# Kernel tuning notes

Measured on AMD Instinct MI355X. Metric: run time of the kernel, lower is better.

Reference implementation:

```python
import jax, jax.numpy as jnp
import numpy as np

TOP_K = 2


def setup_inputs() -> dict:
    key = jax.random.key(0)
    ks = jax.random.split(key, 8)
    B, S, D, E = 4, 2048, 768, 8
    F = 4 * D
    scale = 0.02
    x = jax.random.normal(ks[0], (B, S, D), dtype=jnp.float32)
    router_w = jax.random.normal(ks[1], (D, E), dtype=jnp.float32) * scale
    router_b = jnp.zeros((E,), dtype=jnp.float32)
    w1 = jax.random.normal(ks[2], (E, D, F), dtype=jnp.float32) * scale
    b1 = jnp.zeros((E, F), dtype=jnp.float32)
    w2 = jax.random.normal(ks[3], (E, F, D), dtype=jnp.float32) * scale
    b2 = jnp.zeros((E, D), dtype=jnp.float32)
    return {"x": x, "router_w": router_w, "router_b": router_b,
            "w1": w1, "b1": b1, "w2": w2, "b2": b2}


def reference(x, router_w, router_b, w1, b1, w2, b2):
    E = w1.shape[0]
    # router: [B,S,E]
    logits = jnp.einsum('bsd,de->bse', x, router_w) + router_b
    probs = jax.nn.softmax(logits, axis=-1)
    top_p, top_i = jax.lax.top_k(probs, TOP_K)          # [B,S,K]
    top_p = top_p / jnp.sum(top_p, axis=-1, keepdims=True)
    # dense combine weights [B,S,E]: renormalized top-k prob if selected else 0
    combine = jnp.sum(jax.nn.one_hot(top_i, E, dtype=x.dtype) * top_p[..., None], axis=-2)
    # loop over small fixed expert count (structurally distinct weight slices)
    out = jnp.zeros_like(x)
    for e in range(E):
        h = jax.nn.gelu(jnp.einsum('bsd,df->bsf', x, w1[e]) + b1[e], approximate=False)
        y = jnp.einsum('bsf,fd->bsd', h, w2[e]) + b2[e]
        out = out + combine[..., e:e + 1] * y
    return out
```

## Files before the change

### kernel.cpp

```cpp
#include <hip/hip_runtime.h>
#include <hip/hip_bf16.h>
#include <math.h>

#define TOKENS 8192
#define Dm 768
#define Fm 3072
#define Em 8
#define BK 64

typedef __attribute__((ext_vector_type(8))) short short8v;
typedef __attribute__((ext_vector_type(4))) short short4v;
typedef __attribute__((ext_vector_type(4))) float f32x4;

__device__ inline short f2b(float f) {
  __hip_bfloat16 h = __float2bfloat16(f);
  return *reinterpret_cast<short*>(&h);
}

__device__ inline void async16(short* lds, const short* g) {
  __builtin_amdgcn_global_load_lds((const __attribute__((address_space(1))) void*)g,
                                   (__attribute__((address_space(3))) void*)lds, 16, 0, 0);
}

__global__ __launch_bounds__(256) void cvt_tr_kernel(const float* __restrict__ in,
                                                     short* __restrict__ out, int R, int C) {
  __shared__ short tile[64][68];
  size_t eoff = (size_t)blockIdx.z * R * C;
  const float* inp = in + eoff;
  short* outp = out + eoff;
  int tc = blockIdx.x * 64, tr = blockIdx.y * 64;
  {
    int row = threadIdx.x >> 2;
    int cch = (threadIdx.x & 3) * 16;
    const float* src = inp + (size_t)(tr + row) * C + tc + cch;
    #pragma unroll
    for (int q = 0; q < 4; q++) {
      float4 v = *(const float4*)(src + q * 4);
      tile[row][cch + q * 4 + 0] = f2b(v.x);
      tile[row][cch + q * 4 + 1] = f2b(v.y);
      tile[row][cch + q * 4 + 2] = f2b(v.z);
      tile[row][cch + q * 4 + 3] = f2b(v.w);
    }
  }
  __syncthreads();
  {
    int c = threadIdx.x >> 2;
    int rch = (threadIdx.x & 3) * 16;
    short tmp[16];
    #pragma unroll
    for (int i = 0; i < 16; i++) tmp[i] = tile[rch + i][c];
    short* dst = outp + (size_t)(tc + c) * R + tr + rch;
    *(short8v*)(dst) = *(short8v*)(tmp);
    *(short8v*)(dst + 8) = *(short8v*)(tmp + 8);
  }
}

__global__ __launch_bounds__(256) void router_kernel(
    const float* __restrict__ x, const float* __restrict__ rw,
    const float* __restrict__ rb, short* __restrict__ xb,
    int2* __restrict__ meta_e, float2* __restrict__ meta_p) {
  int wave = threadIdx.x >> 6;
  int lane = threadIdx.x & 63;
  int t = blockIdx.x * 4 + wave;
  if (t >= TOKENS) return;
  const float* xr = x + (size_t)t * Dm;
  short* xbr = xb + (size_t)t * Dm;
  float acc[Em];
  #pragma unroll
  for (int e = 0; e < Em; e++) acc[e] = 0.f;
  #pragma unroll
  for (int i = 0; i < 3; i++) {
    int d = i * 256 + lane * 4;
    float4 v = *(const float4*)(xr + d);
    short4v s;
    s[0] = f2b(v.x); s[1] = f2b(v.y); s[2] = f2b(v.z); s[3] = f2b(v.w);
    *(short4v*)(xbr + d) = s;
    #pragma unroll
    for (int j = 0; j < 4; j++) {
      float xv = (j == 0) ? v.x : (j == 1) ? v.y : (j == 2) ? v.z : v.w;
      const float4* rwp = (const float4*)(rw + (size_t)(d + j) * Em);
      float4 a = rwp[0], b = rwp[1];
      acc[0] += xv * a.x; acc[1] += xv * a.y; acc[2] += xv * a.z; acc[3] += xv * a.w;
      acc[4] += xv * b.x; acc[5] += xv * b.y; acc[6] += xv * b.z; acc[7] += xv * b.w;
    }
  }
  #pragma unroll
  for (int e = 0; e < Em; e++) {
    float v = acc[e];
    #pragma unroll
    for (int s = 32; s > 0; s >>= 1) v += __shfl_xor(v, s);
    acc[e] = v + rb[e];
  }
  int i1 = 0; float m1 = acc[0];
  #pragma unroll
  for (int e = 1; e < Em; e++) if (acc[e] > m1) { m1 = acc[e]; i1 = e; }
  int i2 = -1; float m2 = -1e30f;
  #pragma unroll
  for (int e = 0; e < Em; e++) if (e != i1 && acc[e] > m2) { m2 = acc[e]; i2 = e; }
  float tt = expf(m2 - m1);
  float p0 = 1.f / (1.f + tt);
  float p1 = tt / (1.f + tt);
  if (lane == 0) {
    meta_e[t] = make_int2(i1, i2);
    meta_p[t] = make_float2(p0, p1);
  }
}

__global__ __launch_bounds__(256) void scatter_kernel(
    const int2* __restrict__ meta_e, int* __restrict__ cnt,
    int* __restrict__ list, int4* __restrict__ meta_i) {
  __shared__ int lcnt[Em];
  __shared__ int gbase[Em];
  int t = blockIdx.x * 256 + threadIdx.x;
  if (threadIdx.x < Em) lcnt[threadIdx.x] = 0;
  __syncthreads();
  int2 e = meta_e[t];
  int r0 = atomicAdd(&lcnt[e.x], 1);
  int r1 = atomicAdd(&lcnt[e.y], 1);
  __syncthreads();
  if (threadIdx.x < Em) gbase[threadIdx.x] = atomicAdd(&cnt[threadIdx.x], lcnt[threadIdx.x]);
  __syncthreads();
  int s0 = gbase[e.x] + r0;
  int s1 = gbase[e.y] + r1;
  list[e.x * TOKENS + s0] = t;
  list[e.y * TOKENS + s1] = t;
  meta_i[t] = make_int4(e.x, s0, e.y, s1);
}

__global__ void prefix_kernel(const int* __restrict__ cnt, int* __restrict__ hoffs,
                              int2* __restrict__ table, int* __restrict__ ntab) {
  if (threadIdx.x == 0) {
    int s = 0, k = 0;
    for (int e = 0; e < Em; e++) {
      hoffs[e] = s;
      int c = cnt[e];
      for (int mb = 0; mb < c; mb += 128) table[k++] = make_int2(e, mb);
      s += c;
    }
    ntab[0] = k;
  }
}

template <int MODE>
__global__ __launch_bounds__(256, 3) void moe_gemm_kernel(
    const short* __restrict__ Abase, const short* __restrict__ Wt,
    const float* __restrict__ bias, short* __restrict__ Hout,
    float* __restrict__ Yout, const int* __restrict__ cnt,
    const int* __restrict__ hoffs, const int* __restrict__ list,
    const int2* __restrict__ table, const int* __restrict__ ntab,
    int Ndim, int Kdim) {
  int ti = blockIdx.y;
  if (ti >= ntab[0]) return;
  int2 te = table[ti];
  int e = te.x, mbase = te.y;
  int count = cnt[e], ho = hoffs[e];
  int n0 = blockIdx.x * 128;

  __shared__ short As[128 * 64];
  __shared__ short Bs[128 * 64];
  __shared__ int rid_s[128];

  int tid = threadIdx.x;
  if (MODE == 0) {
    if (tid < 128) {
      int rc = mbase + tid; if (rc > count - 1) rc = count - 1;
      rid_s[tid] = list[e * TOKENS + rc];
    }
  }
  __syncthreads();

  const short* We = Wt + (size_t)e * Ndim * Kdim;
  const short* aptr[4];
  const short* bptr[4];
  #pragma unroll
  for (int q = 0; q < 4; q++) {
    int r = q * 32 + (tid >> 3);
    int g = (tid & 7) ^ (r & 7);
    size_t grow;
    if (MODE == 0) {
      grow = (size_t)rid_s[r] * Kdim;
    } else {
      int rr = mbase + r; if (rr > count - 1) rr = count - 1;
      grow = (size_t)(ho + rr) * Kdim;
    }
    aptr[q] = Abase + grow + g * 8;
    bptr[q] = We + (size_t)(n0 + r) * Kdim + g * 8;
  }
  int w = tid >> 6;
  int NT = Kdim / BK;

  f32x4 acc[4][4] = {};
  int lane = tid & 63;
  int wm = w >> 1, wn = w & 1;
  int lr = lane & 15, lh = lane >> 4;
  int rsw = lr & 7;

  for (int t = 0; t < NT; t++) {
    #pragma unroll
    for (int q = 0; q < 4; q++) {
      async16(&As[q * 2048 + w * 512], aptr[q]); aptr[q] += BK;
      async16(&Bs[q * 2048 + w * 512], bptr[q]); bptr[q] += BK;
    }
    __syncthreads();
    #pragma unroll
    for (int kk = 0; kk < 2; kk++) {
      short8v a[4], b[4];
      #pragma unroll
      for (int m = 0; m < 4; m++)
        a[m] = *(const short8v*)&As[(wm * 64 + m * 16 + lr) * 64 + ((kk * 4 + lh) ^ rsw) * 8];
      #pragma unroll
      for (int n = 0; n < 4; n++)
        b[n] = *(const short8v*)&Bs[(wn * 64 + n * 16 + lr) * 64 + ((kk * 4 + lh) ^ rsw) * 8];
      #pragma unroll
      for (int m = 0; m < 4; m++)
        #pragma unroll
        for (int n = 0; n < 4; n++)
          acc[m][n] = __builtin_amdgcn_mfma_f32_16x16x32_bf16(a[m], b[n], acc[m][n], 0, 0, 0);
    }
    __syncthreads();
  }

  if (MODE == 0) {
    const float* be = bias + (size_t)e * Ndim;
    #pragma unroll
    for (int m = 0; m < 4; m++) {
      #pragma unroll
      for (int j = 0; j < 4; j++) {
        int r = wm * 64 + m * 16 + lh * 4 + j;
        if (mbase + r < count) {
          size_t rowoff = (size_t)(ho + mbase + r) * Ndim;
          #pragma unroll
          for (int n = 0; n < 4; n++) {
            int colg = n0 + wn * 64 + n * 16 + lr;
            float val = acc[m][n][j] + be[colg];
            float z = val * 0.70710678118654752f;
            float az = fabsf(z);
            float tt = __fdividef(1.f, fmaf(0.3275911f, az, 1.f));
            float poly = fmaf(fmaf(fmaf(fmaf(1.061405429f, tt, -1.453152027f), tt,
                              1.421413741f), tt, -0.284496736f), tt, 0.254829592f) * tt;
            float er = 1.f - poly * __expf(-az * az);
            er = z < 0.f ? -er : er;
            val = 0.5f * val * (1.f + er);
            Hout[rowoff + colg] = f2b(val);
          }
        }
      }
    }
  } else {
    #pragma unroll
    for (int m = 0; m < 4; m++) {
      #pragma unroll
      for (int j = 0; j < 4; j++) {
        int r = wm * 64 + m * 16 + lh * 4 + j;
        if (mbase + r < count) {
          float* yrow = Yout + (size_t)(ho + mbase + r) * Ndim;
          #pragma unroll
          for (int n = 0; n < 4; n++) {
            int colg = n0 + wn * 64 + n * 16 + lr;
            yrow[colg] = acc[m][n][j];
          }
        }
      }
    }
  }
}

__global__ __launch_bounds__(256) void combine_kernel(
    const float* __restrict__ Y, const float* __restrict__ b2,
    const int* __restrict__ hoffs, const int4* __restrict__ meta_i,
    const float2* __restrict__ meta_p, float* __restrict__ out) {
  int wave = threadIdx.x >> 6;
  int lane = threadIdx.x & 63;
  int t = blockIdx.x * 4 + wave;
  if (t >= TOKENS) return;
  int4 mi = meta_i[t];
  float2 mp = meta_p[t];
  const float4* y0 = (const float4*)(Y + (size_t)(hoffs[mi.x] + mi.y) * Dm);
  const float4* y1 = (const float4*)(Y + (size_t)(hoffs[mi.z] + mi.w) * Dm);
  const float4* ba = (const float4*)(b2 + (size_t)mi.x * Dm);
  const float4* bb = (const float4*)(b2 + (size_t)mi.z * Dm);
  float4* orow = (float4*)(out + (size_t)t * Dm);
  #pragma unroll
  for (int i = 0; i < 3; i++) {
    int idx = lane + 64 * i;
    float4 v0 = y0[idx], v1 = y1[idx], a = ba[idx], b = bb[idx];
    float4 o;
    o.x = mp.x * (v0.x + a.x) + mp.y * (v1.x + b.x);
    o.y = mp.x * (v0.y + a.y) + mp.y * (v1.y + b.y);
    o.z = mp.x * (v0.z + a.z) + mp.y * (v1.z + b.z);
    o.w = mp.x * (v0.w + a.w) + mp.y * (v1.w + b.w);
    orow[idx] = o;
  }
}

extern "C" void kernel_launch(void* const* d_in, const int* in_sizes, int n_in,
                              void* d_out, int out_size, void* d_ws, size_t ws_size,
                              hipStream_t stream) {
  const float* x  = (const float*)d_in[0];
  const float* rw = (const float*)d_in[1];
  const float* rb = (const float*)d_in[2];
  const float* w1 = (const float*)d_in[3];
  const float* b1 = (const float*)d_in[4];
  const float* w2 = (const float*)d_in[5];
  const float* b2 = (const float*)d_in[6];
  float* out = (float*)d_out;
  char* ws = (char*)d_ws;

  const size_t off_cnt    = 0;
  const size_t off_hoffs  = 64;
  const size_t off_ntab   = 128;
  const size_t off_table  = 192;
  const size_t off_list   = 2048;
  const size_t off_meta_i = off_list + (size_t)Em * TOKENS * 4;
  const size_t off_meta_p = off_meta_i + (size_t)TOKENS * 16;
  const size_t off_meta_e = off_meta_p + (size_t)TOKENS * 8;
  const size_t off_xbf    = off_meta_e + (size_t)TOKENS * 8;
  const size_t off_w1t    = off_xbf + (size_t)TOKENS * Dm * 2;
  const size_t off_w2t    = off_w1t + (size_t)Em * Dm * Fm * 2;
  const size_t off_h      = off_w2t + (size_t)Em * Fm * Dm * 2;
  const size_t needed     = off_h + (size_t)2 * TOKENS * Fm * 2;
  if (ws_size < needed) return;

  int*    cnt    = (int*)(ws + off_cnt);
  int*    hoffs  = (int*)(ws + off_hoffs);
  int*    ntab   = (int*)(ws + off_ntab);
  int2*   table  = (int2*)(ws + off_table);
  int*    list   = (int*)(ws + off_list);
  int4*   meta_i = (int4*)(ws + off_meta_i);
  float2* meta_p = (float2*)(ws + off_meta_p);
  int2*   meta_e = (int2*)(ws + off_meta_e);
  short*  xbf    = (short*)(ws + off_xbf);
  short*  w1t    = (short*)(ws + off_w1t);
  short*  w2t    = (short*)(ws + off_w2t);
  short*  h      = (short*)(ws + off_h);
  float*  y      = (float*)(ws + off_xbf);

  hipMemsetAsync(cnt, 0, 32, stream);
  cvt_tr_kernel<<<dim3(Fm / 64, Dm / 64, Em), 256, 0, stream>>>(w1, w1t, Dm, Fm);
  cvt_tr_kernel<<<dim3(Dm / 64, Fm / 64, Em), 256, 0, stream>>>(w2, w2t, Fm, Dm);
  router_kernel<<<TOKENS / 4, 256, 0, stream>>>(x, rw, rb, xbf, meta_e, meta_p);
  scatter_kernel<<<TOKENS / 256, 256, 0, stream>>>(meta_e, cnt, list, meta_i);
  prefix_kernel<<<1, 64, 0, stream>>>(cnt, hoffs, table, ntab);
  moe_gemm_kernel<0><<<dim3(Fm / 128, 136), 256, 0, stream>>>(
      xbf, w1t, b1, h, nullptr, cnt, hoffs, list, table, ntab, Fm, Dm);
  moe_gemm_kernel<1><<<dim3(Dm / 128, 136), 256, 0, stream>>>(
      h, w2t, nullptr, nullptr, y, cnt, hoffs, list, table, ntab, Dm, Fm);
  combine_kernel<<<TOKENS / 4, 256, 0, stream>>>(y, b2, hoffs, meta_i, meta_p, out);
}
```

Before: 364.0 us.

## Enlarge MoE GEMM tiles, double-buffer LDS, and fuse combine via atomic scatter

Grows the grouped GEMM tile from 128x128 to 256x256 with 512-thread blocks, adds double-buffered async LDS staging, and remaps a 1D grid to spread work across XCDs. The combine kernel is removed. The router pre-writes the bias-weighted output, and the second GEMM atomically adds the probability-weighted results straight into the output rows. This cuts the Y intermediate round-trip and one kernel launch, and raises reuse per tile. It costs fp32 atomics, more padding waste on the larger M tiles, 128 KB of LDS per block, and higher register pressure.

```diff
diff --git a/kernel.cpp b/kernel.cpp
--- a/kernel.cpp
+++ b/kernel.cpp
@@ -7,6 +7,7 @@
 #define Fm 3072
 #define Em 8
 #define BK 64
+#define MT_MAX 71
 
 typedef __attribute__((ext_vector_type(8))) short short8v;
 typedef __attribute__((ext_vector_type(4))) short short4v;
@@ -57,7 +58,8 @@
 
 __global__ __launch_bounds__(256) void router_kernel(
     const float* __restrict__ x, const float* __restrict__ rw,
-    const float* __restrict__ rb, short* __restrict__ xb,
+    const float* __restrict__ rb, const float* __restrict__ b2,
+    short* __restrict__ xb, float* __restrict__ out,
     int2* __restrict__ meta_e, float2* __restrict__ meta_p) {
   int wave = threadIdx.x >> 6;
   int lane = threadIdx.x & 63;
@@ -100,6 +102,18 @@
   float tt = expf(m2 - m1);
   float p0 = 1.f / (1.f + tt);
   float p1 = tt / (1.f + tt);
+  const float4* ba = (const float4*)(b2 + (size_t)i1 * Dm);
+  const float4* bb = (const float4*)(b2 + (size_t)i2 * Dm);
+  float4* orow = (float4*)(out + (size_t)t * Dm);
+  #pragma unroll
+  for (int i = 0; i < 3; i++) {
+    int idx = lane + 64 * i;
+    float4 a = ba[idx], b = bb[idx];
+    float4 o;
+    o.x = p0 * a.x + p1 * b.x; o.y = p0 * a.y + p1 * b.y;
+    o.z = p0 * a.z + p1 * b.z; o.w = p0 * a.w + p1 * b.w;
+    orow[idx] = o;
+  }
   if (lane == 0) {
     meta_e[t] = make_int2(i1, i2);
     meta_p[t] = make_float2(p0, p1);
@@ -107,14 +121,15 @@
 }
 
 __global__ __launch_bounds__(256) void scatter_kernel(
-    const int2* __restrict__ meta_e, int* __restrict__ cnt,
-    int* __restrict__ list, int4* __restrict__ meta_i) {
+    const int2* __restrict__ meta_e, const float2* __restrict__ meta_p,
+    int* __restrict__ cnt, int* __restrict__ list, float* __restrict__ wlist) {
   __shared__ int lcnt[Em];
   __shared__ int gbase[Em];
   int t = blockIdx.x * 256 + threadIdx.x;
   if (threadIdx.x < Em) lcnt[threadIdx.x] = 0;
   __syncthreads();
   int2 e = meta_e[t];
+  float2 p = meta_p[t];
   int r0 = atomicAdd(&lcnt[e.x], 1);
   int r1 = atomicAdd(&lcnt[e.y], 1);
   __syncthreads();
@@ -122,9 +137,8 @@
   __syncthreads();
   int s0 = gbase[e.x] + r0;
   int s1 = gbase[e.y] + r1;
-  list[e.x * TOKENS + s0] = t;
-  list[e.y * TOKENS + s1] = t;
-  meta_i[t] = make_int4(e.x, s0, e.y, s1);
+  list[e.x * TOKENS + s0] = t;  wlist[e.x * TOKENS + s0] = p.x;
+  list[e.y * TOKENS + s1] = t;  wlist[e.y * TOKENS + s1] = p.y;
 }
 
 __global__ void prefix_kernel(const int* __restrict__ cnt, int* __restrict__ hoffs,
@@ -134,38 +148,42 @@
     for (int e = 0; e < Em; e++) {
       hoffs[e] = s;
       int c = cnt[e];
-      for (int mb = 0; mb < c; mb += 128) table[k++] = make_int2(e, mb);
+      for (int mb = 0; mb < c; mb += 256) table[k++] = make_int2(e, mb);
       s += c;
     }
     ntab[0] = k;
   }
 }
 
-template <int MODE>
-__global__ __launch_bounds__(256, 3) void moe_gemm_kernel(
+template <int MODE, int NB>
+__global__ __launch_bounds__(512, 2) void moe_gemm_kernel(
     const short* __restrict__ Abase, const short* __restrict__ Wt,
     const float* __restrict__ bias, short* __restrict__ Hout,
-    float* __restrict__ Yout, const int* __restrict__ cnt,
+    float* __restrict__ Out, const int* __restrict__ cnt,
     const int* __restrict__ hoffs, const int* __restrict__ list,
-    const int2* __restrict__ table, const int* __restrict__ ntab,
-    int Ndim, int Kdim) {
-  int ti = blockIdx.y;
+    const float* __restrict__ wlist, const int2* __restrict__ table,
+    const int* __restrict__ ntab, int Ndim, int Kdim) {
+  int nwg = gridDim.x;
+  int orig = blockIdx.x;
+  int q8 = nwg >> 3, r8 = nwg & 7, xcd = orig & 7;
+  int wg = (xcd < r8 ? xcd * (q8 + 1) : r8 * (q8 + 1) + (xcd - r8) * q8) + (orig >> 3);
+  int ti = wg / NB, nt = wg % NB;
   if (ti >= ntab[0]) return;
   int2 te = table[ti];
   int e = te.x, mbase = te.y;
   int count = cnt[e], ho = hoffs[e];
-  int n0 = blockIdx.x * 128;
-
-  __shared__ short As[128 * 64];
-  __shared__ short Bs[128 * 64];
-  __shared__ int rid_s[128];
+  int n0 = nt * 256;
+
+  __shared__ short As[2][256 * 64];
+  __shared__ short Bs[2][256 * 64];
+  __shared__ int rid_s[256];
+  __shared__ float pw_s[256];
 
   int tid = threadIdx.x;
-  if (MODE == 0) {
-    if (tid < 128) {
-      int rc = mbase + tid; if (rc > count - 1) rc = count - 1;
-      rid_s[tid] = list[e * TOKENS + rc];
-    }
+  if (tid < 256) {
+    int rc = mbase + tid; if (rc > count - 1) rc = count - 1;
+    rid_s[tid] = list[e * TOKENS + rc];
+    pw_s[tid] = wlist[e * TOKENS + rc];
   }
   __syncthreads();
 
@@ -174,7 +192,7 @@
   const short* bptr[4];
   #pragma unroll
   for (int q = 0; q < 4; q++) {
-    int r = q * 32 + (tid >> 3);
+    int r = q * 64 + (tid >> 3);
     int g = (tid & 7) ^ (r & 7);
     size_t grow;
     if (MODE == 0) {
@@ -187,46 +205,57 @@
     bptr[q] = We + (size_t)(n0 + r) * Kdim + g * 8;
   }
   int w = tid >> 6;
+
+  #define STAGE(s)                                             \
+    {                                                          \
+      _Pragma("unroll")                                        \
+      for (int q = 0; q < 4; q++) {                            \
+        async16(&As[s][q * 4096 + w * 512], aptr[q]); aptr[q] += BK; \
+        async16(&Bs[s][q * 4096 + w * 512], bptr[q]); bptr[q] += BK; \
+      }                                                        \
+      __builtin_amdgcn_sched_barrier(0);                       \
+    }
+
   int NT = Kdim / BK;
-
-  f32x4 acc[4][4] = {};
+  f32x4 acc[8][4] = {};
   int lane = tid & 63;
-  int wm = w >> 1, wn = w & 1;
+  int wm = (tid >> 6) >> 2, wn = (tid >> 6) & 3;
   int lr = lane & 15, lh = lane >> 4;
   int rsw = lr & 7;
 
+  STAGE(0);
+  __syncthreads();
   for (int t = 0; t < NT; t++) {
-    #pragma unroll
-    for (int q = 0; q < 4; q++) {
-      async16(&As[q * 2048 + w * 512], aptr[q]); aptr[q] += BK;
-      async16(&Bs[q * 2048 + w * 512], bptr[q]); bptr[q] += BK;
-    }
-    __syncthreads();
+    int cur = t & 1;
+    if (t + 1 < NT) STAGE(cur ^ 1);
+    const short* Ab = As[cur];
+    const short* Bb = Bs[cur];
     #pragma unroll
     for (int kk = 0; kk < 2; kk++) {
-      short8v a[4], b[4];
-      #pragma unroll
-      for (int m = 0; m < 4; m++)
-        a[m] = *(const short8v*)&As[(wm * 64 + m * 16 + lr) * 64 + ((kk * 4 + lh) ^ rsw) * 8];
+      short8v a[8], b[4];
+      #pragma unroll
+      for (int m = 0; m < 8; m++)
+        a[m] = *(const short8v*)&Ab[(wm * 128 + m * 16 + lr) * 64 + ((kk * 4 + lh) ^ rsw) * 8];
       #pragma unroll
       for (int n = 0; n < 4; n++)
-        b[n] = *(const short8v*)&Bs[(wn * 64 + n * 16 + lr) * 64 + ((kk * 4 + lh) ^ rsw) * 8];
-      #pragma unroll
-      for (int m = 0; m < 4; m++)
+        b[n] = *(const short8v*)&Bb[(wn * 64 + n * 16 + lr) * 64 + ((kk * 4 + lh) ^ rsw) * 8];
+      #pragma unroll
+      for (int m = 0; m < 8; m++)
         #pragma unroll
         for (int n = 0; n < 4; n++)
           acc[m][n] = __builtin_amdgcn_mfma_f32_16x16x32_bf16(a[m], b[n], acc[m][n], 0, 0, 0);
     }
     __syncthreads();
   }
+  #undef STAGE
 
   if (MODE == 0) {
     const float* be = bias + (size_t)e * Ndim;
     #pragma unroll
-    for (int m = 0; m < 4; m++) {
+    for (int m = 0; m < 8; m++) {
       #pragma unroll
       for (int j = 0; j < 4; j++) {
-        int r = wm * 64 + m * 16 + lh * 4 + j;
+        int r = wm * 128 + m * 16 + lh * 4 + j;
         if (mbase + r < count) {
           size_t rowoff = (size_t)(ho + mbase + r) * Ndim;
           #pragma unroll
@@ -248,48 +277,21 @@
     }
   } else {
     #pragma unroll
-    for (int m = 0; m < 4; m++) {
+    for (int m = 0; m < 8; m++) {
       #pragma unroll
       for (int j = 0; j < 4; j++) {
-        int r = wm * 64 + m * 16 + lh * 4 + j;
+        int r = wm * 128 + m * 16 + lh * 4 + j;
         if (mbase + r < count) {
-          float* yrow = Yout + (size_t)(ho + mbase + r) * Ndim;
+          float* orow = Out + (size_t)rid_s[r] * Dm;
+          float p = pw_s[r];
           #pragma unroll
           for (int n = 0; n < 4; n++) {
             int colg = n0 + wn * 64 + n * 16 + lr;
-            yrow[colg] = acc[m][n][j];
+            atomicAdd(&orow[colg], p * acc[m][n][j]);
           }
         }
       }
     }
-  }
-}
-
-__global__ __launch_bounds__(256) void combine_kernel(
-    const float* __restrict__ Y, const float* __restrict__ b2,
-    const int* __restrict__ hoffs, const int4* __restrict__ meta_i,
-    const float2* __restrict__ meta_p, float* __restrict__ out) {
-  int wave = threadIdx.x >> 6;
-  int lane = threadIdx.x & 63;
-  int t = blockIdx.x * 4 + wave;
-  if (t >= TOKENS) return;
-  int4 mi = meta_i[t];
-  float2 mp = meta_p[t];
-  const float4* y0 = (const float4*)(Y + (size_t)(hoffs[mi.x] + mi.y) * Dm);
-  const float4* y1 = (const float4*)(Y + (size_t)(hoffs[mi.z] + mi.w) * Dm);
-  const float4* ba = (const float4*)(b2 + (size_t)mi.x * Dm);
-  const float4* bb = (const float4*)(b2 + (size_t)mi.z * Dm);
-  float4* orow = (float4*)(out + (size_t)t * Dm);
-  #pragma unroll
-  for (int i = 0; i < 3; i++) {
-    int idx = lane + 64 * i;
-    float4 v0 = y0[idx], v1 = y1[idx], a = ba[idx], b = bb[idx];
-    float4 o;
-    o.x = mp.x * (v0.x + a.x) + mp.y * (v1.x + b.x);
-    o.y = mp.x * (v0.y + a.y) + mp.y * (v1.y + b.y);
-    o.z = mp.x * (v0.z + a.z) + mp.y * (v1.z + b.z);
-    o.w = mp.x * (v0.w + a.w) + mp.y * (v1.w + b.w);
-    orow[idx] = o;
   }
 }
 
@@ -311,10 +313,10 @@
   const size_t off_ntab   = 128;
   const size_t off_table  = 192;
   const size_t off_list   = 2048;
-  const size_t off_meta_i = off_list + (size_t)Em * TOKENS * 4;
-  const size_t off_meta_p = off_meta_i + (size_t)TOKENS * 16;
-  const size_t off_meta_e = off_meta_p + (size_t)TOKENS * 8;
-  const size_t off_xbf    = off_meta_e + (size_t)TOKENS * 8;
+  const size_t off_wlist  = off_list + (size_t)Em * TOKENS * 4;
+  const size_t off_meta_e = off_wlist + (size_t)Em * TOKENS * 4;
+  const size_t off_meta_p = off_meta_e + (size_t)TOKENS * 8;
+  const size_t off_xbf    = off_meta_p + (size_t)TOKENS * 8;
   const size_t off_w1t    = off_xbf + (size_t)TOKENS * Dm * 2;
   const size_t off_w2t    = off_w1t + (size_t)Em * Dm * Fm * 2;
   const size_t off_h      = off_w2t + (size_t)Em * Fm * Dm * 2;
@@ -326,24 +328,22 @@
   int*    ntab   = (int*)(ws + off_ntab);
   int2*   table  = (int2*)(ws + off_table);
   int*    list   = (int*)(ws + off_list);
-  int4*   meta_i = (int4*)(ws + off_meta_i);
+  float*  wlist  = (float*)(ws + off_wlist);
+  int2*   meta_e = (int2*)(ws + off_meta_e);
   float2* meta_p = (float2*)(ws + off_meta_p);
-  int2*   meta_e = (int2*)(ws + off_meta_e);
   short*  xbf    = (short*)(ws + off_xbf);
   short*  w1t    = (short*)(ws + off_w1t);
   short*  w2t    = (short*)(ws + off_w2t);
   short*  h      = (short*)(ws + off_h);
-  float*  y      = (float*)(ws + off_xbf);
 
   hipMemsetAsync(cnt, 0, 32, stream);
   cvt_tr_kernel<<<dim3(Fm / 64, Dm / 64, Em), 256, 0, stream>>>(w1, w1t, Dm, Fm);
   cvt_tr_kernel<<<dim3(Dm / 64, Fm / 64, Em), 256, 0, stream>>>(w2, w2t, Fm, Dm);
-  router_kernel<<<TOKENS / 4, 256, 0, stream>>>(x, rw, rb, xbf, meta_e, meta_p);
-  scatter_kernel<<<TOKENS / 256, 256, 0, stream>>>(meta_e, cnt, list, meta_i);
+  router_kernel<<<TOKENS / 4, 256, 0, stream>>>(x, rw, rb, b2, xbf, out, meta_e, meta_p);
+  scatter_kernel<<<TOKENS / 256, 256, 0, stream>>>(meta_e, meta_p, cnt, list, wlist);
   prefix_kernel<<<1, 64, 0, stream>>>(cnt, hoffs, table, ntab);
-  moe_gemm_kernel<0><<<dim3(Fm / 128, 136), 256, 0, stream>>>(
-      xbf, w1t, b1, h, nullptr, cnt, hoffs, list, table, ntab, Fm, Dm);
-  moe_gemm_kernel<1><<<dim3(Dm / 128, 136), 256, 0, stream>>>(
-      h, w2t, nullptr, nullptr, y, cnt, hoffs, list, table, ntab, Dm, Fm);
-  combine_kernel<<<TOKENS / 4, 256, 0, stream>>>(y, b2, hoffs, meta_i, meta_p, out);
-}
+  moe_gemm_kernel<0, Fm / 256><<<MT_MAX * (Fm / 256), 512, 0, stream>>>(
+      xbf, w1t, b1, h, nullptr, cnt, hoffs, list, wlist, table, ntab, Fm, Dm);
+  moe_gemm_kernel<1, Dm / 256><<<MT_MAX * (Dm / 256), 512, 0, stream>>>(
+      h, w2t, nullptr, nullptr, out, cnt, hoffs, list, wlist, table, ntab, Dm, Fm);
+}
```

Result: slower. 381.4 us (+4.8%).
